# Kernel optimization log

Measured on AMD Instinct MI355X. Metric: run time of the kernel, lower is better.

## Reference

```python
import jax, jax.numpy as jnp
import numpy as np

B, N, C = 256, 196, 768
H, HD = 12, 64          # num_heads, head_dim
WS = 14                 # window side, N = WS*WS
EPS = 1e-6


def setup_inputs() -> dict:
    key = jax.random.key(0)
    ks = jax.random.split(key, 7)
    s = 0.02
    return {
        "x": jax.random.normal(ks[0], (B, N, C), jnp.float32),
        "w_qkv": jax.random.normal(ks[1], (C, 3 * C), jnp.float32) * s,
        "pos_enc": jax.random.normal(ks[2], (1, N, C), jnp.float32) * s,
        "dwc_w": jax.random.normal(ks[3], (HD, 1, 5, 5), jnp.float32) * s,
        "dwc_b": jax.random.normal(ks[4], (HD,), jnp.float32) * s,
        "w_proj": jax.random.normal(ks[5], (C, C), jnp.float32) * s,
        "b_proj": jax.random.normal(ks[6], (C,), jnp.float32) * s,
    }


def _heads(t):
    # (B, N, C) -> (B*H, N, HD)   ['b n (h c) -> (b h) n c']
    return t.reshape(B, N, H, HD).transpose(0, 2, 1, 3).reshape(B * H, N, HD)


def reference(x, w_qkv, pos_enc, dwc_w, dwc_b, w_proj, b_proj):
    qkv = (x @ w_qkv).reshape(B, N, 3, C)
    q, k, v = qkv[:, :, 0], qkv[:, :, 1], qkv[:, :, 2]
    k = k + pos_enc
    # ReLU kernel feature map
    q = jax.nn.relu(q)
    k = jax.nn.relu(k)
    q, k, v = _heads(q), _heads(k), _heads(v)          # (BH, N, HD) each, fp32
    # normalizer z_i = 1 / (q_i . sum_j k_j + eps)
    z = 1.0 / (jnp.einsum("bic,bc->bi", q, k.sum(axis=1)) + EPS)
    # kv-first order (i*j*(c+d) > c*d*(i+j) for N=196, HD=64)
    kv = jnp.einsum("bjc,bjd->bcd", k, v)              # (BH, HD, HD)
    out = jnp.einsum("bic,bcd,bi->bid", q, kv, z)      # (BH, N, HD)
    # depthwise conv positional mixing on v
    fm = v.transpose(0, 2, 1).reshape(B * H, HD, WS, WS)  # 'b (w h) c -> b c w h'
    fm = jax.lax.conv_general_dilated(
        fm, dwc_w, window_strides=(1, 1), padding="SAME",
        dimension_numbers=("NCHW", "OIHW", "NCHW"), feature_group_count=HD,
    ) + dwc_b[None, :, None, None]
    fm = fm.reshape(B * H, HD, N).transpose(0, 2, 1)   # 'b c w h -> b (w h) c'
    out = out + fm
    # '(b h) n c -> b n (h c)'
    out = out.reshape(B, H, N, HD).transpose(0, 2, 1, 3).reshape(B, N, C)
    return out @ w_proj + b_proj
```

## Files before the change

kernel.cpp:

```cpp
#include <hip/hip_runtime.h>

typedef _Float16 half8_t __attribute__((ext_vector_type(8)));
typedef _Float16 half4_t __attribute__((ext_vector_type(4)));
typedef float f32x4 __attribute__((ext_vector_type(4)));

#define MFMA16(a, b, c) __builtin_amdgcn_mfma_f32_16x16x32_f16((a), (b), (c), 0, 0, 0)

typedef const unsigned int __attribute__((address_space(1)))* gas_ptr;
typedef unsigned int __attribute__((address_space(3)))* las_ptr;

__device__ __forceinline__ void gload16(const void* g, void* l) {
    __builtin_amdgcn_global_load_lds((gas_ptr)g, (las_ptr)l, 16, 0, 0);
}

__device__ __forceinline__ int xcd_swizzle(int bid, int nwg) {
    int xcd = bid & 7, i = bid >> 3;
    int q = nwg >> 3, r = nwg & 7;
    return (xcd < r ? xcd * (q + 1) : r * (q + 1) + (xcd - r) * q) + i;
}


__global__ void cvt_f2h_kernel(const float* __restrict__ in, _Float16* __restrict__ out, int n4) {
    int stride = gridDim.x * blockDim.x;
    for (int i = blockIdx.x * blockDim.x + threadIdx.x; i < n4; i += stride) {
        f32x4 v = *(const f32x4*)(in + (size_t)4 * i);
        half4_t h;
        h[0] = (_Float16)v[0]; h[1] = (_Float16)v[1];
        h[2] = (_Float16)v[2]; h[3] = (_Float16)v[3];
        *(half4_t*)(out + (size_t)4 * i) = h;
    }
}

__global__ void transpose768_kernel(const float* __restrict__ in, _Float16* __restrict__ out, int ncols) {
    int idx = blockIdx.x * 256 + threadIdx.x;
    int total = ncols * 768;
    if (idx < total) {
        int j = idx / 768;
        int k = idx - j * 768;
        out[idx] = (_Float16)in[(size_t)k * ncols + j];
    }
}


#define STG(buf, kof)                                                             \
    {                                                                             \
        _Float16* Ad = lds + (buf) * 12288 + wave * 512;                          \
        _Float16* Bd = lds + (buf) * 12288 + 4096 + wave * 512;                   \
        gload16(Arow + (kof), Ad);                                                \
        gload16(Brow + (kof), Bd);                                                \
        gload16(Brow + (kof) + 98304, Bd + 4096);                                 \
    }

__device__ __forceinline__ void run_gemm128x256(const _Float16* __restrict__ A,
                                                const _Float16* __restrict__ Bt,
                                                int mbase, int nbase,
                                                _Float16* lds,
                                                f32x4 (&acc)[4][4]) {
    const int tid = threadIdx.x;
    const int lane = tid & 63;
    const int wave = tid >> 6;
    const int wr = wave >> 2;
    const int wc = wave & 3;
    const int l15 = lane & 15;
    const int l4 = lane >> 4;
    const int rsw = ((l4 ^ ((l15 >> 1) & 3)) << 3);
    const int ksw = (((tid & 3) ^ ((tid >> 3) & 3)) << 3);

    #pragma unroll
    for (int mi = 0; mi < 4; ++mi)
        #pragma unroll
        for (int ni = 0; ni < 4; ++ni)
            acc[mi][ni] = (f32x4){0.f, 0.f, 0.f, 0.f};

    const _Float16* Arow = A + (size_t)(mbase + (tid >> 2)) * 768 + ksw;
    const _Float16* Brow = Bt + (size_t)(nbase + (tid >> 2)) * 768 + ksw;

    STG(0, 0)
    __syncthreads();

    #pragma unroll 2
    for (int kt = 0; kt < 24; ++kt) {
        const int buf = kt & 1;
        if (kt < 23) STG(buf ^ 1, (kt + 1) * 32)

        const _Float16* Ac = lds + buf * 12288;
        const _Float16* Bc = Ac + 4096;
        half8_t a[4], b[4];
        #pragma unroll
        for (int mi = 0; mi < 4; ++mi)
            a[mi] = *(const half8_t*)(Ac + (wr * 64 + mi * 16 + l15) * 32 + rsw);
        #pragma unroll
        for (int ni = 0; ni < 4; ++ni)
            b[ni] = *(const half8_t*)(Bc + (wc * 64 + ni * 16 + l15) * 32 + rsw);
        #pragma unroll
        for (int mi = 0; mi < 4; ++mi)
            #pragma unroll
            for (int ni = 0; ni < 4; ++ni)
                acc[mi][ni] = MFMA16(a[mi], b[ni], acc[mi][ni]);
        __syncthreads();
    }
}

__global__ __launch_bounds__(512, 4) void gemm_qkv_kernel(
    const _Float16* __restrict__ xh, const _Float16* __restrict__ wqkvT,
    const float* __restrict__ pos_enc,
    _Float16* __restrict__ qh, _Float16* __restrict__ khT, _Float16* __restrict__ vhT) {
    __shared__ _Float16 lds[24576];
    int wgid = xcd_swizzle(blockIdx.x, 392 * 9);
    int mtile = wgid / 9, ntile = wgid - mtile * 9;
    f32x4 acc[4][4];
    run_gemm128x256(xh, wqkvT, mtile * 128, ntile * 256, lds, acc);

    const int tid = threadIdx.x;
    const int lane = tid & 63;
    const int wave = tid >> 6;
    const int wr = wave >> 2;
    const int wc = wave & 3;
    const int l15 = lane & 15;
    const int l4 = lane >> 4;

    const int s = ntile / 3;
    const int cb = (ntile - s * 3) * 256 + wc * 64;

    if (s == 0) {
        #pragma unroll
        for (int mi = 0; mi < 4; ++mi) {
            #pragma unroll
            for (int ni = 0; ni < 4; ++ni) {
                int c = cb + ni * 16 + l15;
                int h = c >> 6, d = c & 63;
                #pragma unroll
                for (int r = 0; r < 4; ++r) {
                    int gr = mtile * 128 + wr * 64 + mi * 16 + l4 * 4 + r;
                    int b = gr / 196;
                    int n = gr - b * 196;
                    qh[((size_t)(b * 12 + h) * 196 + n) * 64 + d] =
                        (_Float16)fmaxf(acc[mi][ni][r], 0.f);
                }
            }
        }
    } else {
        _Float16* dstT = (s == 1) ? khT : vhT;
        #pragma unroll
        for (int mi = 0; mi < 4; ++mi) {
            int gr0 = mtile * 128 + wr * 64 + mi * 16 + l4 * 4;
            int b = gr0 / 196, n0 = gr0 - b * 196;
            #pragma unroll
            for (int ni = 0; ni < 4; ++ni) {
                int c = cb + ni * 16 + l15;
                int h = c >> 6, d = c & 63;
                half4_t w;
                #pragma unroll
                for (int r = 0; r < 4; ++r) {
                    float v = acc[mi][ni][r];
                    if (s == 1) { v += pos_enc[(n0 + r) * 768 + c]; v = fmaxf(v, 0.f); }
                    w[r] = (_Float16)v;
                }
                *(half4_t*)(dstT + ((size_t)(b * 12 + h) * 64 + d) * 196 + n0) = w;
            }
        }
    }
}

__global__ __launch_bounds__(512, 4) void gemm_proj_kernel(
    const _Float16* __restrict__ fused, const _Float16* __restrict__ wprojT,
    const float* __restrict__ b_proj, float* __restrict__ out) {
    __shared__ _Float16 lds[24576];
    int wgid = xcd_swizzle(blockIdx.x, 392 * 3);
    int mtile = wgid / 3, ntile = wgid - mtile * 3;
    f32x4 acc[4][4];
    run_gemm128x256(fused, wprojT, mtile * 128, ntile * 256, lds, acc);

    const int tid = threadIdx.x;
    const int lane = tid & 63;
    const int wave = tid >> 6;
    const int wr = wave >> 2;
    const int wc = wave & 3;
    const int l15 = lane & 15;
    const int l4 = lane >> 4;

    #pragma unroll
    for (int mi = 0; mi < 4; ++mi) {
        #pragma unroll
        for (int ni = 0; ni < 4; ++ni) {
            int gc = ntile * 256 + wc * 64 + ni * 16 + l15;
            float bp = b_proj[gc];
            #pragma unroll
            for (int r = 0; r < 4; ++r) {
                int gr = mtile * 128 + wr * 64 + mi * 16 + l4 * 4 + r;
                out[(size_t)gr * 768 + gc] = acc[mi][ni][r] + bp;
            }
        }
    }
}

__global__ __launch_bounds__(512, 4) void attn_fused_kernel(
    const _Float16* __restrict__ qh, const _Float16* __restrict__ khT,
    const _Float16* __restrict__ vhT,
    const float* __restrict__ dwc_w, const float* __restrict__ dwc_b,
    _Float16* __restrict__ fused) {
    __shared__ _Float16 k_t[64 * 232];
    __shared__ _Float16 v_t[64 * 232];
    __shared__ _Float16 kv_l[64 * 64];
    __shared__ float ksum_p[512];
    __shared__ float ksum[64];
    __shared__ float zz[196];

    int bh = blockIdx.x;
    int bb = bh / 12, hh = bh - bb * 12;
    int tid = threadIdx.x;
    int lane = tid & 63, wave = tid >> 6;
    int l15 = lane & 15, l4 = lane >> 4;
    size_t base = (size_t)bh * 12544;

    for (int s = tid; s < 1856; s += 512) {
        int c = s / 29, g = s - c * 29;
        half8_t kk = {0, 0, 0, 0, 0, 0, 0, 0}, vv = {0, 0, 0, 0, 0, 0, 0, 0};
        const _Float16* kp = khT + base + c * 196 + g * 8;
        const _Float16* vp = vhT + base + c * 196 + g * 8;
        if (g < 24) {
            kk = *(const half8_t*)kp; vv = *(const half8_t*)vp;
        } else if (g == 24) {
            half4_t k4 = *(const half4_t*)kp, v4 = *(const half4_t*)vp;
            kk[0] = k4[0]; kk[1] = k4[1]; kk[2] = k4[2]; kk[3] = k4[3];
            vv[0] = v4[0]; vv[1] = v4[1]; vv[2] = v4[2]; vv[3] = v4[3];
        }
        *(half8_t*)(k_t + c * 232 + g * 8) = kk;
        *(half8_t*)(v_t + c * 232 + g * 8) = vv;
    }
    __syncthreads();

    {
        int ct = wave >> 1, dt0 = (wave & 1) * 2;
        f32x4 acc0 = {0.f, 0.f, 0.f, 0.f}, acc1 = {0.f, 0.f, 0.f, 0.f};
        #pragma unroll
        for (int ks = 0; ks < 7; ++ks) {
            half8_t a  = *(const half8_t*)(k_t + (ct * 16 + l15) * 232 + ks * 32 + l4 * 8);
            half8_t b0 = *(const half8_t*)(v_t + (dt0 * 16 + l15) * 232 + ks * 32 + l4 * 8);
            half8_t b1 = *(const half8_t*)(v_t + (dt0 * 16 + 16 + l15) * 232 + ks * 32 + l4 * 8);
            acc0 = MFMA16(a, b0, acc0);
            acc1 = MFMA16(a, b1, acc1);
        }
        half4_t h0, h1;
        #pragma unroll
        for (int r = 0; r < 4; ++r) { h0[r] = (_Float16)acc0[r]; h1[r] = (_Float16)acc1[r]; }
        int slot = ct * 2 + (l4 >> 1), sub = (l4 & 1) * 4;
        int d0 = dt0 * 16 + l15, d1 = d0 + 16;
        *(half4_t*)(kv_l + d0 * 64 + (((slot ^ (d0 & 7)) << 3) + sub)) = h0;
        *(half4_t*)(kv_l + d1 * 64 + (((slot ^ (d1 & 7)) << 3) + sub)) = h1;
    }
    {
        int n0 = wave * 25;
        int n1 = (n0 + 25 < 196) ? (n0 + 25) : 196;
        float s = 0.f;
        for (int n = n0; n < n1; ++n) s += (float)k_t[lane * 232 + n];
        ksum_p[wave * 64 + lane] = s;
    }
    __syncthreads();
    if (tid < 64) {
        float s = 0.f;
        #pragma unroll
        for (int w = 0; w < 8; ++w) s += ksum_p[w * 64 + tid];
        ksum[tid] = s;
    }
    __syncthreads();
    if (tid < 196) {
        const _Float16* qrow = qh + base + tid * 64;
        float s = 0.f;
        #pragma unroll
        for (int c8 = 0; c8 < 8; ++c8) {
            half8_t qv = *(const half8_t*)(qrow + c8 * 8);
            #pragma unroll
            for (int j = 0; j < 8; ++j) s += (float)qv[j] * ksum[c8 * 8 + j];
        }
        zz[tid] = 1.0f / (s + 1e-6f);
    }
    __syncthreads();

    for (int t = wave; t < 52; t += 8) {
        int mt = t >> 2, dt = t & 3;
        int d = dt * 16 + l15;
        f32x4 acc = {0.f, 0.f, 0.f, 0.f};
        const _Float16* qrow = qh + base + (mt * 16 + l15) * 64;
        half8_t a0 = *(const half8_t*)(qrow + l4 * 8);
        half8_t a1 = *(const half8_t*)(qrow + 32 + l4 * 8);
        half8_t b0 = *(const half8_t*)(kv_l + d * 64 + ((l4 ^ (d & 7)) << 3));
        half8_t b1 = *(const half8_t*)(kv_l + d * 64 + (((l4 + 4) ^ (d & 7)) << 3));
        acc = MFMA16(a0, b0, acc);
        acc = MFMA16(a1, b1, acc);

        float bd = dwc_b[d];
        float wc[25];
        #pragma unroll
        for (int j2 = 0; j2 < 25; ++j2) wc[j2] = dwc_w[d * 25 + j2];

        #pragma unroll
        for (int r = 0; r < 4; ++r) {
            int i = mt * 16 + l4 * 4 + r;
            if (i < 196) {
                int y = i / 14, x2 = i - y * 14;
                float cacc = bd;
                #pragma unroll
                for (int ky = 0; ky < 5; ++ky) {
                    int yy = y + ky - 2;
                    bool oky = (unsigned)yy < 14u;
                    #pragma unroll
                    for (int kx = 0; kx < 5; ++kx) {
                        int xx = x2 + kx - 2;
                        if (oky && (unsigned)xx < 14u)
                            cacc += (float)v_t[d * 232 + (yy * 14 + xx)] * wc[ky * 5 + kx];
                    }
                }
                float res = acc[r] * zz[i] + cacc;
                fused[((size_t)bb * 196 + i) * 768 + hh * 64 + d] = (_Float16)res;
            }
        }
    }
}


extern "C" void kernel_launch(void* const* d_in, const int* in_sizes, int n_in,
                              void* d_out, int out_size, void* d_ws, size_t ws_size,
                              hipStream_t stream) {
    const float* x       = (const float*)d_in[0];
    const float* w_qkv   = (const float*)d_in[1];
    const float* pos_enc = (const float*)d_in[2];
    const float* dwc_w   = (const float*)d_in[3];
    const float* dwc_b   = (const float*)d_in[4];
    const float* w_proj  = (const float*)d_in[5];
    const float* b_proj  = (const float*)d_in[6];

    const size_t NEEDED = 340574208;
    if (ws_size < NEEDED) return;

    char* ws = (char*)d_ws;
    _Float16* xh     = (_Float16*)(ws + 0);
    _Float16* fused  = xh;
    _Float16* wqkvT  = (_Float16*)(ws + 77070336);
    _Float16* wprojT = (_Float16*)(ws + 80609280);
    _Float16* qh     = (_Float16*)(ws + 81788928);
    _Float16* khT    = (_Float16*)(ws + 158859264);
    _Float16* vhT    = (_Float16*)(ws + 235929600);

    cvt_f2h_kernel<<<4096, 256, 0, stream>>>(x, xh, 9633792);
    transpose768_kernel<<<(2304 * 768 + 255) / 256, 256, 0, stream>>>(w_qkv, wqkvT, 2304);
    transpose768_kernel<<<(768 * 768 + 255) / 256, 256, 0, stream>>>(w_proj, wprojT, 768);
    gemm_qkv_kernel<<<392 * 9, 512, 0, stream>>>(xh, wqkvT, pos_enc, qh, khT, vhT);
    attn_fused_kernel<<<3072, 512, 0, stream>>>(qh, khT, vhT, dwc_w, dwc_b, fused);
    gemm_proj_kernel<<<392 * 3, 512, 0, stream>>>(fused, wprojT, b_proj, (float*)d_out);
}
```

Before: 660.2 us.

## Switch GEMMs to 128x128 tiles with BK=64 single-buffered LDS and 256 threads

Replaces the 128x256 double-buffered GEMM core (BK=32, 512 threads) with a 128x128 tile, BK=64 single-buffered core run by 4 waves, using a new XOR swizzle for LDS reads. Grids double for both the QKV and projection GEMMs, and the epilogues are remapped to the new wave layout. This gives smaller per-block LDS and more blocks to improve occupancy and load balance. In exchange it drops the overlap between global loads and compute that double buffering provided, and it lowers B-tile reuse per block.

```diff
diff --git a/kernel.cpp b/kernel.cpp
--- a/kernel.cpp
+++ b/kernel.cpp
@@ -42,29 +42,30 @@
 }
 
 
-#define STG(buf, kof)                                                             \
+#define STG128(kof)                                                               \
     {                                                                             \
-        _Float16* Ad = lds + (buf) * 12288 + wave * 512;                          \
-        _Float16* Bd = lds + (buf) * 12288 + 4096 + wave * 512;                   \
-        gload16(Arow + (kof), Ad);                                                \
-        gload16(Brow + (kof), Bd);                                                \
-        gload16(Brow + (kof) + 98304, Bd + 4096);                                 \
-    }
-
-__device__ __forceinline__ void run_gemm128x256(const _Float16* __restrict__ A,
-                                                const _Float16* __restrict__ Bt,
-                                                int mbase, int nbase,
-                                                _Float16* lds,
-                                                f32x4 (&acc)[4][4]) {
+        _Pragma("unroll")                                                         \
+        for (int i = 0; i < 4; ++i) {                                             \
+            gload16(ArowS + (kof) + i * 24576, As + wave * 512 + i * 2048);       \
+            gload16(BrowS + (kof) + i * 24576, Bs + wave * 512 + i * 2048);       \
+        }                                                                         \
+    }
+
+__device__ __forceinline__ void run_gemm128(const _Float16* __restrict__ A,
+                                            const _Float16* __restrict__ Bt,
+                                            int mbase, int nbase,
+                                            _Float16* As, _Float16* Bs,
+                                            f32x4 (&acc)[4][4]) {
     const int tid = threadIdx.x;
     const int lane = tid & 63;
     const int wave = tid >> 6;
-    const int wr = wave >> 2;
-    const int wc = wave & 3;
+    const int wm = (wave >> 1) * 64;
+    const int wn = (wave & 1) * 64;
     const int l15 = lane & 15;
     const int l4 = lane >> 4;
-    const int rsw = ((l4 ^ ((l15 >> 1) & 3)) << 3);
-    const int ksw = (((tid & 3) ^ ((tid >> 3) & 3)) << 3);
+    const int rs = l15 & 7;
+    const int srow = lane >> 3;
+    const int ssl = ((lane & 7) ^ srow) << 3;
 
     #pragma unroll
     for (int mi = 0; mi < 4; ++mi)
@@ -72,55 +73,54 @@
         for (int ni = 0; ni < 4; ++ni)
             acc[mi][ni] = (f32x4){0.f, 0.f, 0.f, 0.f};
 
-    const _Float16* Arow = A + (size_t)(mbase + (tid >> 2)) * 768 + ksw;
-    const _Float16* Brow = Bt + (size_t)(nbase + (tid >> 2)) * 768 + ksw;
-
-    STG(0, 0)
-    __syncthreads();
-
-    #pragma unroll 2
-    for (int kt = 0; kt < 24; ++kt) {
-        const int buf = kt & 1;
-        if (kt < 23) STG(buf ^ 1, (kt + 1) * 32)
-
-        const _Float16* Ac = lds + buf * 12288;
-        const _Float16* Bc = Ac + 4096;
-        half8_t a[4], b[4];
-        #pragma unroll
-        for (int mi = 0; mi < 4; ++mi)
-            a[mi] = *(const half8_t*)(Ac + (wr * 64 + mi * 16 + l15) * 32 + rsw);
-        #pragma unroll
-        for (int ni = 0; ni < 4; ++ni)
-            b[ni] = *(const half8_t*)(Bc + (wc * 64 + ni * 16 + l15) * 32 + rsw);
-        #pragma unroll
-        for (int mi = 0; mi < 4; ++mi)
+    const _Float16* ArowS = A + (size_t)(mbase + wave * 8 + srow) * 768 + ssl;
+    const _Float16* BrowS = Bt + (size_t)(nbase + wave * 8 + srow) * 768 + ssl;
+
+    for (int kt = 0; kt < 12; ++kt) {
+        STG128(kt * 64)
+        __syncthreads();
+        #pragma unroll
+        for (int h = 0; h < 2; ++h) {
+            half8_t a[4], b[4];
+            #pragma unroll
+            for (int mi = 0; mi < 4; ++mi)
+                a[mi] = *(const half8_t*)(As + (wm + mi * 16 + l15) * 64 +
+                                          (((h * 4 + l4) ^ rs) << 3));
             #pragma unroll
             for (int ni = 0; ni < 4; ++ni)
-                acc[mi][ni] = MFMA16(a[mi], b[ni], acc[mi][ni]);
+                b[ni] = *(const half8_t*)(Bs + (wn + ni * 16 + l15) * 64 +
+                                          (((h * 4 + l4) ^ rs) << 3));
+            #pragma unroll
+            for (int mi = 0; mi < 4; ++mi)
+                #pragma unroll
+                for (int ni = 0; ni < 4; ++ni)
+                    acc[mi][ni] = MFMA16(a[mi], b[ni], acc[mi][ni]);
+        }
         __syncthreads();
     }
 }
 
-__global__ __launch_bounds__(512, 4) void gemm_qkv_kernel(
+__global__ __launch_bounds__(256, 4) void gemm_qkv_kernel(
     const _Float16* __restrict__ xh, const _Float16* __restrict__ wqkvT,
     const float* __restrict__ pos_enc,
     _Float16* __restrict__ qh, _Float16* __restrict__ khT, _Float16* __restrict__ vhT) {
-    __shared__ _Float16 lds[24576];
-    int wgid = xcd_swizzle(blockIdx.x, 392 * 9);
-    int mtile = wgid / 9, ntile = wgid - mtile * 9;
+    __shared__ _Float16 As[8192];
+    __shared__ _Float16 Bs[8192];
+    int wgid = xcd_swizzle(blockIdx.x, 392 * 18);
+    int mtile = wgid / 18, ntile = wgid - mtile * 18;
     f32x4 acc[4][4];
-    run_gemm128x256(xh, wqkvT, mtile * 128, ntile * 256, lds, acc);
+    run_gemm128(xh, wqkvT, mtile * 128, ntile * 128, As, Bs, acc);
 
     const int tid = threadIdx.x;
     const int lane = tid & 63;
     const int wave = tid >> 6;
-    const int wr = wave >> 2;
-    const int wc = wave & 3;
+    const int wm = (wave >> 1) * 64;
+    const int wn = (wave & 1) * 64;
     const int l15 = lane & 15;
     const int l4 = lane >> 4;
 
-    const int s = ntile / 3;
-    const int cb = (ntile - s * 3) * 256 + wc * 64;
+    const int s = ntile / 6;
+    const int cb = (ntile - s * 6) * 128 + wn;
 
     if (s == 0) {
         #pragma unroll
@@ -131,7 +131,7 @@
                 int h = c >> 6, d = c & 63;
                 #pragma unroll
                 for (int r = 0; r < 4; ++r) {
-                    int gr = mtile * 128 + wr * 64 + mi * 16 + l4 * 4 + r;
+                    int gr = mtile * 128 + wm + mi * 16 + l4 * 4 + r;
                     int b = gr / 196;
                     int n = gr - b * 196;
                     qh[((size_t)(b * 12 + h) * 196 + n) * 64 + d] =
@@ -143,7 +143,7 @@
         _Float16* dstT = (s == 1) ? khT : vhT;
         #pragma unroll
         for (int mi = 0; mi < 4; ++mi) {
-            int gr0 = mtile * 128 + wr * 64 + mi * 16 + l4 * 4;
+            int gr0 = mtile * 128 + wm + mi * 16 + l4 * 4;
             int b = gr0 / 196, n0 = gr0 - b * 196;
             #pragma unroll
             for (int ni = 0; ni < 4; ++ni) {
@@ -162,20 +162,21 @@
     }
 }
 
-__global__ __launch_bounds__(512, 4) void gemm_proj_kernel(
+__global__ __launch_bounds__(256, 4) void gemm_proj_kernel(
     const _Float16* __restrict__ fused, const _Float16* __restrict__ wprojT,
     const float* __restrict__ b_proj, float* __restrict__ out) {
-    __shared__ _Float16 lds[24576];
-    int wgid = xcd_swizzle(blockIdx.x, 392 * 3);
-    int mtile = wgid / 3, ntile = wgid - mtile * 3;
+    __shared__ _Float16 As[8192];
+    __shared__ _Float16 Bs[8192];
+    int wgid = xcd_swizzle(blockIdx.x, 392 * 6);
+    int mtile = wgid / 6, ntile = wgid - mtile * 6;
     f32x4 acc[4][4];
-    run_gemm128x256(fused, wprojT, mtile * 128, ntile * 256, lds, acc);
+    run_gemm128(fused, wprojT, mtile * 128, ntile * 128, As, Bs, acc);
 
     const int tid = threadIdx.x;
     const int lane = tid & 63;
     const int wave = tid >> 6;
-    const int wr = wave >> 2;
-    const int wc = wave & 3;
+    const int wm = (wave >> 1) * 64;
+    const int wn = (wave & 1) * 64;
     const int l15 = lane & 15;
     const int l4 = lane >> 4;
 
@@ -183,11 +184,11 @@
     for (int mi = 0; mi < 4; ++mi) {
         #pragma unroll
         for (int ni = 0; ni < 4; ++ni) {
-            int gc = ntile * 256 + wc * 64 + ni * 16 + l15;
+            int gc = ntile * 128 + wn + ni * 16 + l15;
             float bp = b_proj[gc];
             #pragma unroll
             for (int r = 0; r < 4; ++r) {
-                int gr = mtile * 128 + wr * 64 + mi * 16 + l4 * 4 + r;
+                int gr = mtile * 128 + wm + mi * 16 + l4 * 4 + r;
                 out[(size_t)gr * 768 + gc] = acc[mi][ni][r] + bp;
             }
         }
@@ -345,7 +346,7 @@
     cvt_f2h_kernel<<<4096, 256, 0, stream>>>(x, xh, 9633792);
     transpose768_kernel<<<(2304 * 768 + 255) / 256, 256, 0, stream>>>(w_qkv, wqkvT, 2304);
     transpose768_kernel<<<(768 * 768 + 255) / 256, 256, 0, stream>>>(w_proj, wprojT, 768);
-    gemm_qkv_kernel<<<392 * 9, 512, 0, stream>>>(xh, wqkvT, pos_enc, qh, khT, vhT);
+    gemm_qkv_kernel<<<392 * 18, 256, 0, stream>>>(xh, wqkvT, pos_enc, qh, khT, vhT);
     attn_fused_kernel<<<3072, 512, 0, stream>>>(qh, khT, vhT, dwc_w, dwc_b, fused);
-    gemm_proj_kernel<<<392 * 3, 512, 0, stream>>>(fused, wprojT, b_proj, (float*)d_out);
-}
+    gemm_proj_kernel<<<392 * 6, 256, 0, stream>>>(fused, wprojT, b_proj, (float*)d_out);
+}
```

Result: faster. 645.9 us (-2.2%).
